# Kernel tuning notes

Measured on AMD Instinct MI355X. Metric: run time of the kernel, lower is better.

Reference implementation:

```python
import jax, jax.numpy as jnp
import numpy as np

B, T, RNN_DIM, ENC_DIM, ATT_DIM, NFILT, KSIZE = 256, 1024, 1024, 512, 128, 32, 31
PAD = (KSIZE - 1) // 2


def setup_inputs() -> dict:
    key = jax.random.key(0)
    ks = jax.random.split(key, 10)
    attn = jax.random.uniform(ks[3], (B, T), dtype=jnp.float32)
    attn = attn / jnp.sum(attn, axis=1, keepdims=True)  # previous-step alignment (sums to 1)
    return {
        "query": jax.random.normal(ks[0], (B, RNN_DIM), dtype=jnp.float32),
        "memory": jax.random.normal(ks[1], (B, T, ENC_DIM), dtype=jnp.float32),
        "processed_memory": jax.random.normal(ks[2], (B, T, ATT_DIM), dtype=jnp.float32),
        "attn_weights": attn,
        "attn_weights_cum": jax.random.uniform(ks[4], (B, T), dtype=jnp.float32),
        "memory_lengths": jax.random.randint(ks[5], (B,), T // 2, T + 1),
        "conv_w": jax.random.normal(ks[6], (NFILT, 2, KSIZE), dtype=jnp.float32) * 0.1,
        "W_loc": jax.random.normal(ks[7], (ATT_DIM, NFILT), dtype=jnp.float32) * 0.1,
        "W_q": jax.random.normal(ks[8], (ATT_DIM, RNN_DIM), dtype=jnp.float32) * 0.03,
        "v_w": jax.random.normal(ks[9], (1, ATT_DIM), dtype=jnp.float32) * 0.1,
        "v_b": jnp.zeros((1,), dtype=jnp.float32),
    }


def reference(query, memory, processed_memory, attn_weights, attn_weights_cum,
              memory_lengths, conv_w, W_loc, W_q, v_w, v_b):
    Tlen = memory.shape[1]
    # [B, 2, T]: stack prev + cumulative alignments
    cat = jnp.stack([attn_weights, attn_weights_cum], axis=1)
    # location conv: Conv1d(2 -> NFILT, k=31, same padding, no bias) -> [B, NFILT, T]
    loc = jax.lax.conv_general_dilated(
        cat, conv_w, window_strides=(1,), padding=[(PAD, PAD)],
        dimension_numbers=("NCH", "OIH", "NCH"))
    # location_dense: [B, T, ATT_DIM]
    processed_location = jnp.einsum("bct,ac->bta", loc, W_loc)
    # query projection: [B, 1, ATT_DIM]
    processed_query = (query @ W_q.T)[:, None, :]
    # additive energies: v . tanh(q + loc + mem) -> [B, T]
    hidden = jnp.tanh(processed_query + processed_location + processed_memory)
    energies = jnp.einsum("bta,a->bt", hidden, v_w[0]) + v_b[0]
    # mask padded positions (pos >= length) with -inf
    mask = jnp.arange(Tlen)[None, :] >= memory_lengths[:, None]
    energies = jnp.where(mask, -jnp.inf, energies)
    new_attn = jax.nn.softmax(energies, axis=1)
    new_cum = attn_weights_cum + new_attn
    # context: [B, ENC_DIM]
    context = jnp.einsum("bt,bte->be", new_attn, memory)
    return context, new_attn, new_cum
```

## Files before the change

kernel.cpp:

```cpp
#include <hip/hip_runtime.h>
#include <math.h>

#define Bc 256
#define Tc 1024
#define RNN_DIMc 1024
#define ENC_DIMc 512
#define ATT_DIMc 128
#define NFILTc 32
#define KSIZEc 31
#define PADc 15

__device__ __forceinline__ float fast_tanh(float x) {
    x = fminf(15.f, fmaxf(-15.f, x));
    float z = __expf(2.f * x);
    return (z - 1.f) / (z + 1.f);
}

__device__ __forceinline__ float wave_reduce_max(float x) {
#pragma unroll
    for (int off = 32; off > 0; off >>= 1) x = fmaxf(x, __shfl_xor(x, off, 64));
    return x;
}

__device__ __forceinline__ float wave_reduce_sum(float x) {
#pragma unroll
    for (int off = 32; off > 0; off >>= 1) x += __shfl_xor(x, off, 64);
    return x;
}

__global__ __launch_bounds__(1024) void lsa_fused(
    const float* __restrict__ query, const float* __restrict__ memory,
    const float* __restrict__ pm, const float* __restrict__ attn_w,
    const float* __restrict__ cum_w, const int* __restrict__ lens,
    const float* __restrict__ conv_w, const float* __restrict__ W_loc,
    const float* __restrict__ W_q, const float* __restrict__ v_w,
    const float* __restrict__ v_b, float* __restrict__ ctx,
    float* __restrict__ out_attn, float* __restrict__ out_cum) {
    const int b = blockIdx.x;
    const int tid = threadIdx.x;

    __shared__ float s_q[RNN_DIMc];
    __shared__ float s_pq[ATT_DIMc];
    __shared__ float s_win0[Tc + 2 * PADc];
    __shared__ float s_win1[Tc + 2 * PADc];
    __shared__ float s_attn[Tc];
    __shared__ float s_redm[16];
    __shared__ float s_reds[16];
    __shared__ float s_scratch[8][ENC_DIMc];

    if (tid < RNN_DIMc) s_q[tid] = query[b * RNN_DIMc + tid];
    for (int i = tid; i < Tc + 2 * PADc; i += 1024) {
        int tt = i - PADc;
        bool ok = (tt >= 0) && (tt < Tc);
        s_win0[i] = ok ? attn_w[b * Tc + tt] : 0.f;
        s_win1[i] = ok ? cum_w[b * Tc + tt] : 0.f;
    }
    __syncthreads();

    {
        const int a = tid >> 3;
        const int c = tid & 7;
        const float* w = W_q + (size_t)a * RNN_DIMc + c * 128;
        const float* qq = s_q + c * 128;
        float acc = 0.f;
#pragma unroll
        for (int j = 0; j < 128; j += 4) {
            float4 wv = *(const float4*)(w + j);
            acc = fmaf(wv.x, qq[j + 0], acc);
            acc = fmaf(wv.y, qq[j + 1], acc);
            acc = fmaf(wv.z, qq[j + 2], acc);
            acc = fmaf(wv.w, qq[j + 3], acc);
        }
        ((float*)s_scratch)[a * 8 + c] = acc;
    }
    __syncthreads();
    if (tid < ATT_DIMc) {
        const float* p = (const float*)s_scratch + tid * 8;
        s_pq[tid] = p[0] + p[1] + p[2] + p[3] + p[4] + p[5] + p[6] + p[7];
    }
    __syncthreads();

    const int t = tid;
    float e;
    {
        float loc[NFILTc];
#pragma unroll
        for (int f = 0; f < NFILTc; ++f) loc[f] = 0.f;
        for (int k = 0; k < KSIZEc; ++k) {
            const float wa = s_win0[t + k];
            const float wc = s_win1[t + k];
#pragma unroll
            for (int f = 0; f < NFILTc; ++f) {
                loc[f] = fmaf(conv_w[f * (2 * KSIZEc) + k], wa, loc[f]);
                loc[f] = fmaf(conv_w[f * (2 * KSIZEc) + KSIZEc + k], wc, loc[f]);
            }
        }

        const float* pmrow = pm + ((size_t)(b * Tc + t)) * ATT_DIMc;
        e = 0.f;
#pragma unroll 2
        for (int a = 0; a < ATT_DIMc; a += 4) {
            float4 pmv = *(const float4*)(pmrow + a);
            const float* wl = W_loc + a * NFILTc;
            float pl0 = 0.f, pl1 = 0.f, pl2 = 0.f, pl3 = 0.f;
#pragma unroll
            for (int f = 0; f < NFILTc; ++f) {
                float lf = loc[f];
                pl0 = fmaf(wl[f], lf, pl0);
                pl1 = fmaf(wl[NFILTc + f], lf, pl1);
                pl2 = fmaf(wl[2 * NFILTc + f], lf, pl2);
                pl3 = fmaf(wl[3 * NFILTc + f], lf, pl3);
            }
            e = fmaf(v_w[a + 0], fast_tanh(s_pq[a + 0] + pl0 + pmv.x), e);
            e = fmaf(v_w[a + 1], fast_tanh(s_pq[a + 1] + pl1 + pmv.y), e);
            e = fmaf(v_w[a + 2], fast_tanh(s_pq[a + 2] + pl2 + pmv.z), e);
            e = fmaf(v_w[a + 3], fast_tanh(s_pq[a + 3] + pl3 + pmv.w), e);
        }
        e += v_b[0];
        if (t >= lens[b]) e = -INFINITY;
    }

    {
        float m = wave_reduce_max(e);
        if ((tid & 63) == 0) s_redm[tid >> 6] = m;
        __syncthreads();
        float bm = s_redm[0];
#pragma unroll
        for (int j = 1; j < 16; ++j) bm = fmaxf(bm, s_redm[j]);

        float p = __expf(e - bm);
        float s = wave_reduce_sum(p);
        if ((tid & 63) == 0) s_reds[tid >> 6] = s;
        __syncthreads();
        float tot = 0.f;
#pragma unroll
        for (int j = 0; j < 16; ++j) tot += s_reds[j];
        float na = p * (1.f / tot);

        out_attn[b * Tc + t] = na;
        out_cum[b * Tc + t] = s_win1[t + PADc] + na;
        s_attn[t] = na;
    }
    __syncthreads();

    {
        const int tr = tid >> 7;
        const int e4 = (tid & 127) * 4;
        const float* mb = memory + (size_t)b * Tc * ENC_DIMc;
        float4 acc = make_float4(0.f, 0.f, 0.f, 0.f);
#pragma unroll 4
        for (int tt = tr; tt < Tc; tt += 8) {
            const float w = s_attn[tt];
            const float4 mv = *(const float4*)(mb + (size_t)tt * ENC_DIMc + e4);
            acc.x = fmaf(w, mv.x, acc.x);
            acc.y = fmaf(w, mv.y, acc.y);
            acc.z = fmaf(w, mv.z, acc.z);
            acc.w = fmaf(w, mv.w, acc.w);
        }
        *(float4*)&s_scratch[tr][e4] = acc;
    }
    __syncthreads();
    if (tid < ENC_DIMc) {
        float s = 0.f;
#pragma unroll
        for (int j = 0; j < 8; ++j) s += s_scratch[j][tid];
        ctx[b * ENC_DIMc + tid] = s;
    }
}

extern "C" void kernel_launch(void* const* d_in, const int* in_sizes, int n_in,
                              void* d_out, int out_size, void* d_ws, size_t ws_size,
                              hipStream_t stream) {
    const float* query  = (const float*)d_in[0];
    const float* memory = (const float*)d_in[1];
    const float* pm     = (const float*)d_in[2];
    const float* attn_w = (const float*)d_in[3];
    const float* cum_w  = (const float*)d_in[4];
    const int*   lens   = (const int*)d_in[5];
    const float* conv_w = (const float*)d_in[6];
    const float* W_loc  = (const float*)d_in[7];
    const float* W_q    = (const float*)d_in[8];
    const float* v_w    = (const float*)d_in[9];
    const float* v_b    = (const float*)d_in[10];

    float* out      = (float*)d_out;
    float* ctx      = out;
    float* out_attn = out + Bc * ENC_DIMc;
    float* out_cum  = out + Bc * ENC_DIMc + Bc * Tc;

    lsa_fused<<<Bc, 1024, 0, stream>>>(query, memory, pm, attn_w, cum_w, lens,
                                       conv_w, W_loc, W_q, v_w, v_b,
                                       ctx, out_attn, out_cum);
}
```

Baseline: 829.2 us.

## Split query projection into separate kernel, skip masked positions, use nontemporal loads

Moves the query projection into its own small kernel writing to workspace, so the fused kernel no longer computes it behind two block-wide barriers. Energy computation and the context reduction now skip time steps at or beyond each sequence's length. Those steps get zero softmax weight, so the output is unchanged while about a quarter of the memory and processed_memory reads are avoided on average. Streaming loads are marked nontemporal. The cost is an extra kernel launch and a small global round-trip for the projected query.

```diff
diff --git a/kernel.cpp b/kernel.cpp
--- a/kernel.cpp
+++ b/kernel.cpp
@@ -9,6 +9,8 @@
 #define NFILTc 32
 #define KSIZEc 31
 #define PADc 15
+
+typedef float f4v __attribute__((ext_vector_type(4)));
 
 __device__ __forceinline__ float fast_tanh(float x) {
     x = fminf(15.f, fmaxf(-15.f, x));
@@ -28,18 +30,37 @@
     return x;
 }
 
+__global__ __launch_bounds__(128) void qproj_k(const float* __restrict__ query,
+                                               const float* __restrict__ W_q,
+                                               float* __restrict__ pq) {
+    const int b = blockIdx.x;
+    __shared__ float q[RNN_DIMc];
+    for (int i = threadIdx.x; i < RNN_DIMc; i += 128) q[i] = query[b * RNN_DIMc + i];
+    __syncthreads();
+    const float* w = W_q + (size_t)threadIdx.x * RNN_DIMc;
+    float acc = 0.f;
+#pragma unroll 4
+    for (int r = 0; r < RNN_DIMc; r += 4) {
+        float4 wv = *(const float4*)(w + r);
+        acc = fmaf(wv.x, q[r + 0], acc);
+        acc = fmaf(wv.y, q[r + 1], acc);
+        acc = fmaf(wv.z, q[r + 2], acc);
+        acc = fmaf(wv.w, q[r + 3], acc);
+    }
+    pq[b * ATT_DIMc + threadIdx.x] = acc;
+}
+
 __global__ __launch_bounds__(1024) void lsa_fused(
-    const float* __restrict__ query, const float* __restrict__ memory,
-    const float* __restrict__ pm, const float* __restrict__ attn_w,
-    const float* __restrict__ cum_w, const int* __restrict__ lens,
-    const float* __restrict__ conv_w, const float* __restrict__ W_loc,
-    const float* __restrict__ W_q, const float* __restrict__ v_w,
-    const float* __restrict__ v_b, float* __restrict__ ctx,
-    float* __restrict__ out_attn, float* __restrict__ out_cum) {
+    const float* __restrict__ memory, const float* __restrict__ pm,
+    const float* __restrict__ attn_w, const float* __restrict__ cum_w,
+    const int* __restrict__ lens, const float* __restrict__ conv_w,
+    const float* __restrict__ W_loc, const float* __restrict__ pq_g,
+    const float* __restrict__ v_w, const float* __restrict__ v_b,
+    float* __restrict__ ctx, float* __restrict__ out_attn, float* __restrict__ out_cum) {
     const int b = blockIdx.x;
     const int tid = threadIdx.x;
+    const int len = lens[b];
 
-    __shared__ float s_q[RNN_DIMc];
     __shared__ float s_pq[ATT_DIMc];
     __shared__ float s_win0[Tc + 2 * PADc];
     __shared__ float s_win1[Tc + 2 * PADc];
@@ -48,7 +69,7 @@
     __shared__ float s_reds[16];
     __shared__ float s_scratch[8][ENC_DIMc];
 
-    if (tid < RNN_DIMc) s_q[tid] = query[b * RNN_DIMc + tid];
+    if (tid < ATT_DIMc) s_pq[tid] = pq_g[b * ATT_DIMc + tid];
     for (int i = tid; i < Tc + 2 * PADc; i += 1024) {
         int tt = i - PADc;
         bool ok = (tt >= 0) && (tt < Tc);
@@ -57,32 +78,9 @@
     }
     __syncthreads();
 
-    {
-        const int a = tid >> 3;
-        const int c = tid & 7;
-        const float* w = W_q + (size_t)a * RNN_DIMc + c * 128;
-        const float* qq = s_q + c * 128;
-        float acc = 0.f;
-#pragma unroll
-        for (int j = 0; j < 128; j += 4) {
-            float4 wv = *(const float4*)(w + j);
-            acc = fmaf(wv.x, qq[j + 0], acc);
-            acc = fmaf(wv.y, qq[j + 1], acc);
-            acc = fmaf(wv.z, qq[j + 2], acc);
-            acc = fmaf(wv.w, qq[j + 3], acc);
-        }
-        ((float*)s_scratch)[a * 8 + c] = acc;
-    }
-    __syncthreads();
-    if (tid < ATT_DIMc) {
-        const float* p = (const float*)s_scratch + tid * 8;
-        s_pq[tid] = p[0] + p[1] + p[2] + p[3] + p[4] + p[5] + p[6] + p[7];
-    }
-    __syncthreads();
-
     const int t = tid;
-    float e;
-    {
+    float e = -INFINITY;
+    if (t < len) {
         float loc[NFILTc];
 #pragma unroll
         for (int f = 0; f < NFILTc; ++f) loc[f] = 0.f;
@@ -97,10 +95,10 @@
         }
 
         const float* pmrow = pm + ((size_t)(b * Tc + t)) * ATT_DIMc;
-        e = 0.f;
+        float acc = 0.f;
 #pragma unroll 2
         for (int a = 0; a < ATT_DIMc; a += 4) {
-            float4 pmv = *(const float4*)(pmrow + a);
+            const f4v pmv = __builtin_nontemporal_load((const f4v*)(pmrow + a));
             const float* wl = W_loc + a * NFILTc;
             float pl0 = 0.f, pl1 = 0.f, pl2 = 0.f, pl3 = 0.f;
 #pragma unroll
@@ -111,13 +109,12 @@
                 pl2 = fmaf(wl[2 * NFILTc + f], lf, pl2);
                 pl3 = fmaf(wl[3 * NFILTc + f], lf, pl3);
             }
-            e = fmaf(v_w[a + 0], fast_tanh(s_pq[a + 0] + pl0 + pmv.x), e);
-            e = fmaf(v_w[a + 1], fast_tanh(s_pq[a + 1] + pl1 + pmv.y), e);
-            e = fmaf(v_w[a + 2], fast_tanh(s_pq[a + 2] + pl2 + pmv.z), e);
-            e = fmaf(v_w[a + 3], fast_tanh(s_pq[a + 3] + pl3 + pmv.w), e);
+            acc = fmaf(v_w[a + 0], fast_tanh(s_pq[a + 0] + pl0 + pmv.x), acc);
+            acc = fmaf(v_w[a + 1], fast_tanh(s_pq[a + 1] + pl1 + pmv.y), acc);
+            acc = fmaf(v_w[a + 2], fast_tanh(s_pq[a + 2] + pl2 + pmv.z), acc);
+            acc = fmaf(v_w[a + 3], fast_tanh(s_pq[a + 3] + pl3 + pmv.w), acc);
         }
-        e += v_b[0];
-        if (t >= lens[b]) e = -INFINITY;
+        e = acc + v_b[0];
     }
 
     {
@@ -147,17 +144,17 @@
         const int tr = tid >> 7;
         const int e4 = (tid & 127) * 4;
         const float* mb = memory + (size_t)b * Tc * ENC_DIMc;
-        float4 acc = make_float4(0.f, 0.f, 0.f, 0.f);
+        f4v acc = {0.f, 0.f, 0.f, 0.f};
 #pragma unroll 4
-        for (int tt = tr; tt < Tc; tt += 8) {
+        for (int tt = tr; tt < len; tt += 8) {
             const float w = s_attn[tt];
-            const float4 mv = *(const float4*)(mb + (size_t)tt * ENC_DIMc + e4);
+            const f4v mv = __builtin_nontemporal_load((const f4v*)(mb + (size_t)tt * ENC_DIMc + e4));
             acc.x = fmaf(w, mv.x, acc.x);
             acc.y = fmaf(w, mv.y, acc.y);
             acc.z = fmaf(w, mv.z, acc.z);
             acc.w = fmaf(w, mv.w, acc.w);
         }
-        *(float4*)&s_scratch[tr][e4] = acc;
+        *(f4v*)&s_scratch[tr][e4] = acc;
     }
     __syncthreads();
     if (tid < ENC_DIMc) {
@@ -188,7 +185,10 @@
     float* out_attn = out + Bc * ENC_DIMc;
     float* out_cum  = out + Bc * ENC_DIMc + Bc * Tc;
 
-    lsa_fused<<<Bc, 1024, 0, stream>>>(query, memory, pm, attn_w, cum_w, lens,
-                                       conv_w, W_loc, W_q, v_w, v_b,
+    float* pq = (float*)d_ws;
+
+    qproj_k<<<Bc, 128, 0, stream>>>(query, W_q, pq);
+    lsa_fused<<<Bc, 1024, 0, stream>>>(memory, pm, attn_w, cum_w, lens,
+                                       conv_w, W_loc, pq, v_w, v_b,
                                        ctx, out_attn, out_cum);
 }
```

Result: no change. 818.3 us (-1.3%).
